# Kernel tuning notes

Hardware: AMD Instinct MI355X
Metric: run time of the kernel (lower is better)

Reference implementation:

```python
import jax, jax.numpy as jnp
import numpy as np

V = 2562
DEG = 8
NNZ = V * DEG
B, FIN, FOUT, K = 1, 8, 16, 5
X = Y = Z = 8


def setup_inputs() -> dict:
    key = jax.random.key(0)
    k1, k2, k3, k4, k5 = jax.random.split(key, 5)
    inputs = jax.random.normal(k1, (B, FIN, V, X, Y, Z), dtype=jnp.float32)
    # COO sparse Laplacian: each vertex has DEG entries (valid row indices)
    lap_rows = jnp.repeat(jnp.arange(V, dtype=jnp.int32), DEG)
    lap_cols = jax.random.randint(k2, (NNZ,), 0, V, dtype=jnp.int32)
    lap_vals = jax.random.normal(k3, (NNZ,), dtype=jnp.float32) * 0.1
    std = np.sqrt(2.0 / (FIN * K)).astype(np.float32)
    weight = jax.random.normal(k4, (K, FIN, FOUT), dtype=jnp.float32) * std
    bias = jnp.full((FOUT,), 0.01, dtype=jnp.float32)
    return {"inputs": inputs, "lap_rows": lap_rows, "lap_cols": lap_cols,
            "lap_vals": lap_vals, "weight": weight, "bias": bias}


def _spmv(vals, rows, cols, x):
    # sparse [V,V] @ dense [V,D] via gather + segment_sum
    return jax.ops.segment_sum(vals[:, None] * x[cols], rows, num_segments=V)


def reference(inputs, lap_rows, lap_cols, lap_vals, weight, bias):
    # x0: [V, Fin*B*X*Y*Z]
    x0 = jnp.transpose(inputs, (2, 1, 0, 3, 4, 5)).reshape(V, FIN * B * X * Y * Z)
    xs = [x0]
    if K > 1:
        x1 = _spmv(lap_vals, lap_rows, lap_cols, x0)
        xs.append(x1)
        for _ in range(2, K):
            x2 = 2.0 * _spmv(lap_vals, lap_rows, lap_cols, x1) - x0
            xs.append(x2)
            x0, x1 = x1, x2
    cheb = jnp.stack(xs, 0).reshape(K, V, FIN, B, X, Y, Z)
    # matmul over (K, Fin): out [B, Fout, V, X, Y, Z]
    out = jnp.einsum('kvfbxyz,kfo->bovxyz', cheb, weight)
    out = out + bias[None, :, None, None, None, None]
    return out
```

## Files before the change

### kernel.cpp

```cpp
#include <hip/hip_runtime.h>
#include <hip/hip_bf16.h>
#include <hip/hip_fp16.h>

constexpr int V_    = 2562;
constexpr int DEG_  = 8;
constexpr int FIN_  = 8;
constexpr int FOUT_ = 16;
constexpr int S_    = 512;
constexpr int VS_   = V_ * S_;
constexpr int VP_   = 2564;
constexpr int LSTR  = 12;
constexpr long INT_PLANE = (long)S_ * VP_;
constexpr int TPB   = 1024;
constexpr int NV    = 3;

__device__ __forceinline__ float4 ld4(const float* p) {
    return *reinterpret_cast<const float4*>(p);
}
__device__ __forceinline__ void st4(float* p, float4 v) {
    *reinterpret_cast<float4*>(p) = v;
}
__device__ __forceinline__ unsigned h2bits(__half2 h) {
    union { __half2 h; unsigned u; } c; c.h = h; return c.u;
}
__device__ __forceinline__ __half2 bits2h(unsigned u) {
    union { unsigned u; __half2 h; } c; c.u = u; return c.h;
}
__device__ __forceinline__ unsigned packh2(float e, float o) {
    return h2bits(__halves2half2(__float2half(e), __float2half(o)));
}

__global__ __launch_bounds__(256)
void transpose_k(const float* __restrict__ src, float* __restrict__ dst,
                 int M, int N, long srcZ, long dstZ, int dstStride)
{
    __shared__ float tile[64][65];
    const long zs = (long)blockIdx.z * srcZ;
    const long zd = (long)blockIdx.z * dstZ;
    const int n0 = blockIdx.x * 64;
    const int m0 = blockIdx.y * 64;
    const int t  = threadIdx.x;
    const int q  = t & 15;
    const int r  = t >> 4;

#pragma unroll
    for (int i = 0; i < 4; ++i) {
        const int m = m0 + r + i * 16;
        const int n = n0 + q * 4;
        if (m < M && n < N) {
            const float4 x = ld4(src + zs + (long)m * N + n);
            tile[r + i * 16][q * 4 + 0] = x.x;
            tile[r + i * 16][q * 4 + 1] = x.y;
            tile[r + i * 16][q * 4 + 2] = x.z;
            tile[r + i * 16][q * 4 + 3] = x.w;
        }
    }
    __syncthreads();
#pragma unroll
    for (int i = 0; i < 4; ++i) {
        const int n = n0 + r + i * 16;
        const int m = m0 + q * 4;
        if (n < N && (m + 4) <= dstStride) {
            const float4 x = make_float4(tile[q * 4 + 0][r + i * 16],
                                         tile[q * 4 + 1][r + i * 16],
                                         tile[q * 4 + 2][r + i * 16],
                                         tile[q * 4 + 3][r + i * 16]);
            st4(dst + zd + (long)n * dstStride + m, x);
        }
    }
}

__global__ __launch_bounds__(TPB)
void cheb_rec(const float* __restrict__ inT,
              const int*   __restrict__ cols,
              const float* __restrict__ vals,
              ushort* __restrict__ cheb)
{
    extern __shared__ unsigned cur[];
    const int s2 = blockIdx.x * 2;
    const int t  = threadIdx.x;

    {
        const int f  = t & 7;
        const int cb = t >> 3;
        const float* pe = inT + (long)f * INT_PLANE + (long)s2 * VP_;
        const float* po = pe + VP_;
        for (int c = cb; c < VP_ / 4; c += TPB / 8) {
            const float4 xe = ld4(pe + c * 4);
            const float4 xo = ld4(po + c * 4);
            cur[(c * 4 + 0) * LSTR + f] = packh2(xe.x, xo.x);
            cur[(c * 4 + 1) * LSTR + f] = packh2(xe.y, xo.y);
            cur[(c * 4 + 2) * LSTR + f] = packh2(xe.z, xo.z);
            cur[(c * 4 + 3) * LSTR + f] = packh2(xe.w, xo.w);
        }
    }
    __syncthreads();

    const __half2 two2 = __half2half2(__float2half(2.0f));

    __half2 xp[NV][8];
#pragma unroll
    for (int j = 0; j < NV; ++j) {
        const int v = (t + j * TPB < V_) ? (t + j * TPB) : 0;
        const uint4 lo = *reinterpret_cast<const uint4*>(&cur[v * LSTR]);
        const uint4 hi = *reinterpret_cast<const uint4*>(&cur[v * LSTR + 4]);
        xp[j][0] = bits2h(lo.x); xp[j][1] = bits2h(lo.y);
        xp[j][2] = bits2h(lo.z); xp[j][3] = bits2h(lo.w);
        xp[j][4] = bits2h(hi.x); xp[j][5] = bits2h(hi.y);
        xp[j][6] = bits2h(hi.z); xp[j][7] = bits2h(hi.w);
    }

#pragma unroll 1
    for (int k = 1; k < 5; ++k) {
        __half2 xk[NV][8];
#pragma unroll
        for (int j = 0; j < NV; ++j) {
            const bool valid = (t + j * TPB) < V_;
            const int v = valid ? (t + j * TPB) : 0;
            int off = v * 8;
            asm volatile("" : "+v"(off));
            const int4   ca = *reinterpret_cast<const int4*>(cols + off);
            const int4   cb = *reinterpret_cast<const int4*>(cols + off + 4);
            const float4 wa = ld4(vals + off);
            const float4 wb = ld4(vals + off + 4);
            const int   cc[8] = {ca.x, ca.y, ca.z, ca.w, cb.x, cb.y, cb.z, cb.w};
            const float ww[8] = {wa.x, wa.y, wa.z, wa.w, wb.x, wb.y, wb.z, wb.w};

            __half2 a[8];
#pragma unroll
            for (int e = 0; e < 8; ++e) a[e] = bits2h(0u);
#pragma unroll
            for (int n = 0; n < 8; ++n) {
                const unsigned* p = &cur[cc[n] * LSTR];
                const uint4 lo = *reinterpret_cast<const uint4*>(p);
                const uint4 hi = *reinterpret_cast<const uint4*>(p + 4);
                const __half2 w2 = __half2half2(__float2half(ww[n]));
                a[0] = __hfma2(w2, bits2h(lo.x), a[0]);
                a[1] = __hfma2(w2, bits2h(lo.y), a[1]);
                a[2] = __hfma2(w2, bits2h(lo.z), a[2]);
                a[3] = __hfma2(w2, bits2h(lo.w), a[3]);
                a[4] = __hfma2(w2, bits2h(hi.x), a[4]);
                a[5] = __hfma2(w2, bits2h(hi.y), a[5]);
                a[6] = __hfma2(w2, bits2h(hi.z), a[6]);
                a[7] = __hfma2(w2, bits2h(hi.w), a[7]);
            }
#pragma unroll
            for (int e = 0; e < 8; ++e)
                xk[j][e] = (k == 1) ? a[e]
                                    : __hfma2(two2, a[e], __hneg2(xp[j][e]));

            if (valid) {
                unsigned ue[4], uo[4];
#pragma unroll
                for (int i = 0; i < 4; ++i) {
                    const unsigned b0 = h2bits(xk[j][2 * i]);
                    const unsigned b1 = h2bits(xk[j][2 * i + 1]);
                    ue[i] = __builtin_amdgcn_perm(b1, b0, 0x05040100u);
                    uo[i] = __builtin_amdgcn_perm(b1, b0, 0x07060302u);
                }
                const long base = (((long)(k - 1) * S_ + s2) * V_ + v) * 8;
                *reinterpret_cast<uint4*>(cheb + base) =
                    make_uint4(ue[0], ue[1], ue[2], ue[3]);
                *reinterpret_cast<uint4*>(cheb + base + (long)V_ * 8) =
                    make_uint4(uo[0], uo[1], uo[2], uo[3]);
            }

            if (k < 4) {
                const uint4 lo = *reinterpret_cast<const uint4*>(&cur[v * LSTR]);
                const uint4 hi = *reinterpret_cast<const uint4*>(&cur[v * LSTR + 4]);
                xp[j][0] = bits2h(lo.x); xp[j][1] = bits2h(lo.y);
                xp[j][2] = bits2h(lo.z); xp[j][3] = bits2h(lo.w);
                xp[j][4] = bits2h(hi.x); xp[j][5] = bits2h(hi.y);
                xp[j][6] = bits2h(hi.z); xp[j][7] = bits2h(hi.w);
            }
        }
        if (k < 4) {
            __syncthreads();
#pragma unroll
            for (int j = 0; j < NV; ++j) {
                const int vr = t + j * TPB;
                if (vr < V_) {
                    *reinterpret_cast<uint4*>(&cur[vr * LSTR]) =
                        make_uint4(h2bits(xk[j][0]), h2bits(xk[j][1]),
                                   h2bits(xk[j][2]), h2bits(xk[j][3]));
                    *reinterpret_cast<uint4*>(&cur[vr * LSTR + 4]) =
                        make_uint4(h2bits(xk[j][4]), h2bits(xk[j][5]),
                                   h2bits(xk[j][6]), h2bits(xk[j][7]));
                }
            }
            __syncthreads();
        }
    }
}

__global__ __launch_bounds__(TPB)
void proj(const float* __restrict__ in,
          const ushort* __restrict__ cheb,
          const float* __restrict__ W,
          const float* __restrict__ bias,
          float* __restrict__ out)
{
    extern __shared__ float sm[];
    const int v0 = blockIdx.x * 64;
    const int s0 = blockIdx.y * 16;
    const int t  = threadIdx.x;

    const int tv = t & 63;
    const int ts = t >> 6;
    const int vg = (v0 + tv < V_) ? (v0 + tv) : (V_ - 1);

    int4 ck[4];
#pragma unroll
    for (int k = 0; k < 4; ++k)
        ck[k] = *reinterpret_cast<const int4*>(
            cheb + (((long)k * S_ + (s0 + ts)) * V_ + vg) * 8);

#pragma unroll
    for (int p = 0; p < 2; ++p) {
        const int idx = t + p * TPB;
        const int sq  = idx & 3;
        const int v   = (idx >> 2) & 63;
        const int f   = idx >> 8;
        const int vvg = (v0 + v < V_) ? (v0 + v) : (V_ - 1);
        const float4 x = ld4(in + (long)f * VS_ + (long)vvg * S_ + s0 + sq * 4);
        float* d = &sm[f * 1088 + v * 17 + sq * 4];
        d[0] = x.x; d[1] = x.y; d[2] = x.z; d[3] = x.w;
    }
    __syncthreads();

    float acc[16];
#pragma unroll
    for (int o = 0; o < 16; ++o) acc[o] = bias[o];

#pragma unroll
    for (int f = 0; f < FIN_; ++f) {
        const float xv = sm[f * 1088 + tv * 17 + ts];
#pragma unroll
        for (int o = 0; o < 16; ++o)
            acc[o] = fmaf(W[f * 16 + o], xv, acc[o]);
    }
#pragma unroll
    for (int k = 1; k < 5; ++k) {
        union { int4 q; __half u[8]; } pk;
        pk.q = ck[k - 1];
        float xv[8];
#pragma unroll
        for (int f = 0; f < 8; ++f)
            xv[f] = __half2float(pk.u[f]);
#pragma unroll
        for (int f = 0; f < 8; ++f) {
#pragma unroll
            for (int o = 0; o < 16; ++o)
                acc[o] = fmaf(W[(k * 8 + f) * 16 + o], xv[f], acc[o]);
        }
    }

    __syncthreads();
#pragma unroll
    for (int o = 0; o < 16; ++o)
        sm[o * 1088 + tv * 17 + ts] = acc[o];
    __syncthreads();
#pragma unroll
    for (int p = 0; p < 4; ++p) {
        const int idx = t + p * TPB;
        const int sq  = idx & 3;
        const int v   = (idx >> 2) & 63;
        const int o   = idx >> 8;
        if (v0 + v < V_) {
            const float* r = &sm[o * 1088 + v * 17 + sq * 4];
            st4(out + (long)o * VS_ + (long)(v0 + v) * S_ + s0 + sq * 4,
                make_float4(r[0], r[1], r[2], r[3]));
        }
    }
}

extern "C" void kernel_launch(void* const* d_in, const int* in_sizes, int n_in,
                              void* d_out, int out_size, void* d_ws, size_t ws_size,
                              hipStream_t stream) {
    const float* in   = (const float*)d_in[0];
    const int*   cols = (const int*)d_in[2];
    const float* vals = (const float*)d_in[3];
    const float* W    = (const float*)d_in[4];
    const float* bias = (const float*)d_in[5];
    float* out = (float*)d_out;

    float* inT = out;
    ushort* cheb = (ushort*)d_ws;

    (void)hipFuncSetAttribute((const void*)cheb_rec,
                              hipFuncAttributeMaxDynamicSharedMemorySize,
                              VP_ * LSTR * (int)sizeof(unsigned));
    (void)hipFuncSetAttribute((const void*)proj,
                              hipFuncAttributeMaxDynamicSharedMemorySize,
                              16 * 64 * 17 * (int)sizeof(float));

    transpose_k<<<dim3(8, 41, 8), 256, 0, stream>>>(
        in, inT, V_, S_, (long)VS_, INT_PLANE, VP_);

    cheb_rec<<<dim3(S_ / 2), TPB, VP_ * LSTR * (int)sizeof(unsigned), stream>>>(
        inT, cols, vals, cheb);

    proj<<<dim3(41, 32), TPB, 16 * 64 * 17 * (int)sizeof(float), stream>>>(
        in, cheb, W, bias, out);
}
```

Baseline: 199.9 us.

## Pack transposed input to fp16 pairs and feed x0 from cheb kernel to projection

The transpose kernel now writes fp16 half2-packed pairs of spatial columns instead of fp32, halving the intermediate buffer and removing the pack step in the recurrence kernel's load. When the workspace is large enough, the recurrence kernel also writes x0 in the same fp16 layout as the other Chebyshev terms. A new projection kernel then reads all five terms uniformly and skips the strided fp32 input gather through shared memory. The cost is an extra x0 write and x0 now being rounded to fp16 in the projection, which adds precision loss; a fallback keeps the old four-term path.

Measured after the change: 187.9 us. -6.0%, faster.

```diff
diff --git a/kernel.cpp b/kernel.cpp
--- a/kernel.cpp
+++ b/kernel.cpp
@@ -1,16 +1,16 @@
 #include <hip/hip_runtime.h>
-#include <hip/hip_bf16.h>
 #include <hip/hip_fp16.h>
 
 constexpr int V_    = 2562;
-constexpr int DEG_  = 8;
 constexpr int FIN_  = 8;
 constexpr int FOUT_ = 16;
 constexpr int S_    = 512;
+constexpr int SP_   = 256;
 constexpr int VS_   = V_ * S_;
 constexpr int VP_   = 2564;
 constexpr int LSTR  = 12;
-constexpr long INT_PLANE = (long)S_ * VP_;
+constexpr long PLH  = (long)SP_ * VP_;
+constexpr long PS   = (long)S_ * V_ * 8;
 constexpr int TPB   = 1024;
 constexpr int NV    = 3;
 
@@ -31,24 +31,23 @@
 }
 
 __global__ __launch_bounds__(256)
-void transpose_k(const float* __restrict__ src, float* __restrict__ dst,
-                 int M, int N, long srcZ, long dstZ, int dstStride)
+void transpose_pack(const float* __restrict__ src, unsigned* __restrict__ dst)
 {
     __shared__ float tile[64][65];
-    const long zs = (long)blockIdx.z * srcZ;
-    const long zd = (long)blockIdx.z * dstZ;
+    const int f  = blockIdx.z;
     const int n0 = blockIdx.x * 64;
     const int m0 = blockIdx.y * 64;
     const int t  = threadIdx.x;
     const int q  = t & 15;
     const int r  = t >> 4;
+    const float* sp_ = src + (long)f * VS_;
 
 #pragma unroll
     for (int i = 0; i < 4; ++i) {
         const int m = m0 + r + i * 16;
         const int n = n0 + q * 4;
-        if (m < M && n < N) {
-            const float4 x = ld4(src + zs + (long)m * N + n);
+        if (m < V_) {
+            const float4 x = ld4(sp_ + (long)m * S_ + n);
             tile[r + i * 16][q * 4 + 0] = x.x;
             tile[r + i * 16][q * 4 + 1] = x.y;
             tile[r + i * 16][q * 4 + 2] = x.z;
@@ -56,25 +55,32 @@
         }
     }
     __syncthreads();
-#pragma unroll
-    for (int i = 0; i < 4; ++i) {
-        const int n = n0 + r + i * 16;
-        const int m = m0 + q * 4;
-        if (n < N && (m + 4) <= dstStride) {
-            const float4 x = make_float4(tile[q * 4 + 0][r + i * 16],
-                                         tile[q * 4 + 1][r + i * 16],
-                                         tile[q * 4 + 2][r + i * 16],
-                                         tile[q * 4 + 3][r + i * 16]);
-            st4(dst + zd + (long)n * dstStride + m, x);
+
+#pragma unroll
+    for (int i = 0; i < 2; ++i) {
+        const int idx = t + i * 256;
+        const int vq  = idx & 15;
+        const int sp  = idx >> 4;
+        const int m   = m0 + vq * 4;
+        if (m + 4 <= VP_) {
+            unsigned u[4];
+#pragma unroll
+            for (int e = 0; e < 4; ++e)
+                u[e] = packh2(tile[vq * 4 + e][2 * sp],
+                              tile[vq * 4 + e][2 * sp + 1]);
+            *reinterpret_cast<uint4*>(
+                dst + (long)f * PLH + (long)(n0 / 2 + sp) * VP_ + m) =
+                make_uint4(u[0], u[1], u[2], u[3]);
         }
     }
 }
 
 __global__ __launch_bounds__(TPB)
-void cheb_rec(const float* __restrict__ inT,
+void cheb_rec(const unsigned* __restrict__ inTh,
               const int*   __restrict__ cols,
               const float* __restrict__ vals,
-              ushort* __restrict__ cheb)
+              ushort* __restrict__ chebX1,
+              ushort* __restrict__ x0p)
 {
     extern __shared__ unsigned cur[];
     const int s2 = blockIdx.x * 2;
@@ -83,18 +89,40 @@
     {
         const int f  = t & 7;
         const int cb = t >> 3;
-        const float* pe = inT + (long)f * INT_PLANE + (long)s2 * VP_;
-        const float* po = pe + VP_;
+        const unsigned* pl = inTh + (long)f * PLH + (long)blockIdx.x * VP_;
         for (int c = cb; c < VP_ / 4; c += TPB / 8) {
-            const float4 xe = ld4(pe + c * 4);
-            const float4 xo = ld4(po + c * 4);
-            cur[(c * 4 + 0) * LSTR + f] = packh2(xe.x, xo.x);
-            cur[(c * 4 + 1) * LSTR + f] = packh2(xe.y, xo.y);
-            cur[(c * 4 + 2) * LSTR + f] = packh2(xe.z, xo.z);
-            cur[(c * 4 + 3) * LSTR + f] = packh2(xe.w, xo.w);
-        }
-    }
-    __syncthreads();
+            const uint4 u = *reinterpret_cast<const uint4*>(pl + c * 4);
+            cur[(c * 4 + 0) * LSTR + f] = u.x;
+            cur[(c * 4 + 1) * LSTR + f] = u.y;
+            cur[(c * 4 + 2) * LSTR + f] = u.z;
+            cur[(c * 4 + 3) * LSTR + f] = u.w;
+        }
+    }
+    __syncthreads();
+
+    if (x0p) {
+#pragma unroll
+        for (int j = 0; j < NV; ++j) {
+            const int v = t + j * TPB;
+            if (v < V_) {
+                const uint4 lo = *reinterpret_cast<const uint4*>(&cur[v * LSTR]);
+                const uint4 hi = *reinterpret_cast<const uint4*>(&cur[v * LSTR + 4]);
+                const unsigned p0[4] = { lo.x, lo.z, hi.x, hi.z };
+                const unsigned p1[4] = { lo.y, lo.w, hi.y, hi.w };
+                unsigned ue[4], uo[4];
+#pragma unroll
+                for (int i = 0; i < 4; ++i) {
+                    ue[i] = __builtin_amdgcn_perm(p1[i], p0[i], 0x05040100u);
+                    uo[i] = __builtin_amdgcn_perm(p1[i], p0[i], 0x07060302u);
+                }
+                const long base = ((long)s2 * V_ + v) * 8;
+                *reinterpret_cast<uint4*>(x0p + base) =
+                    make_uint4(ue[0], ue[1], ue[2], ue[3]);
+                *reinterpret_cast<uint4*>(x0p + base + (long)V_ * 8) =
+                    make_uint4(uo[0], uo[1], uo[2], uo[3]);
+            }
+        }
+    }
 
     const __half2 two2 = __half2half2(__float2half(2.0f));
 
@@ -159,9 +187,9 @@
                     uo[i] = __builtin_amdgcn_perm(b1, b0, 0x07060302u);
                 }
                 const long base = (((long)(k - 1) * S_ + s2) * V_ + v) * 8;
-                *reinterpret_cast<uint4*>(cheb + base) =
+                *reinterpret_cast<uint4*>(chebX1 + base) =
                     make_uint4(ue[0], ue[1], ue[2], ue[3]);
-                *reinterpret_cast<uint4*>(cheb + base + (long)V_ * 8) =
+                *reinterpret_cast<uint4*>(chebX1 + base + (long)V_ * 8) =
                     make_uint4(uo[0], uo[1], uo[2], uo[3]);
             }
 
@@ -194,26 +222,83 @@
 }
 
 __global__ __launch_bounds__(TPB)
-void proj(const float* __restrict__ in,
-          const ushort* __restrict__ cheb,
-          const float* __restrict__ W,
-          const float* __restrict__ bias,
-          float* __restrict__ out)
+void proj5(const ushort* __restrict__ cheb,
+           const float* __restrict__ W,
+           const float* __restrict__ bias,
+           float* __restrict__ out)
 {
     extern __shared__ float sm[];
     const int v0 = blockIdx.x * 64;
     const int s0 = blockIdx.y * 16;
     const int t  = threadIdx.x;
-
     const int tv = t & 63;
     const int ts = t >> 6;
     const int vg = (v0 + tv < V_) ? (v0 + tv) : (V_ - 1);
 
+    int4 ck[5];
+#pragma unroll
+    for (int k = 0; k < 5; ++k)
+        ck[k] = *reinterpret_cast<const int4*>(
+            cheb + (long)k * PS + ((long)(s0 + ts) * V_ + vg) * 8);
+
+    float acc[16];
+#pragma unroll
+    for (int o = 0; o < 16; ++o) acc[o] = bias[o];
+
+#pragma unroll
+    for (int k = 0; k < 5; ++k) {
+        union { int4 q; __half u[8]; } pk;
+        pk.q = ck[k];
+        float xf[8];
+#pragma unroll
+        for (int f = 0; f < 8; ++f)
+            xf[f] = __half2float(pk.u[f]);
+#pragma unroll
+        for (int f = 0; f < 8; ++f) {
+#pragma unroll
+            for (int o = 0; o < 16; ++o)
+                acc[o] = fmaf(W[(k * 8 + f) * 16 + o], xf[f], acc[o]);
+        }
+    }
+
+#pragma unroll
+    for (int o = 0; o < 16; ++o)
+        sm[o * 1088 + tv * 17 + ts] = acc[o];
+    __syncthreads();
+#pragma unroll
+    for (int p = 0; p < 4; ++p) {
+        const int idx = t + p * TPB;
+        const int sq  = idx & 3;
+        const int v   = (idx >> 2) & 63;
+        const int o   = idx >> 8;
+        if (v0 + v < V_) {
+            const float* r = &sm[o * 1088 + v * 17 + sq * 4];
+            st4(out + (long)o * VS_ + (long)(v0 + v) * S_ + s0 + sq * 4,
+                make_float4(r[0], r[1], r[2], r[3]));
+        }
+    }
+}
+
+__global__ __launch_bounds__(TPB)
+void proj4(const float* __restrict__ in,
+           const ushort* __restrict__ cheb,
+           const float* __restrict__ W,
+           const float* __restrict__ bias,
+           float* __restrict__ out)
+{
+    extern __shared__ float sm[];
+    const int v0 = blockIdx.x * 64;
+    const int s0 = blockIdx.y * 16;
+    const int t  = threadIdx.x;
+    const int tv = t & 63;
+    const int ts = t >> 6;
+    const int vg = (v0 + tv < V_) ? (v0 + tv) : (V_ - 1);
+
     int4 ck[4];
 #pragma unroll
     for (int k = 0; k < 4; ++k)
         ck[k] = *reinterpret_cast<const int4*>(
-            cheb + (((long)k * S_ + (s0 + ts)) * V_ + vg) * 8);
+            cheb + (long)k * PS + ((long)(s0 + ts) * V_ + vg) * 8);
 
 #pragma unroll
     for (int p = 0; p < 2; ++p) {
@@ -243,15 +328,15 @@
     for (int k = 1; k < 5; ++k) {
         union { int4 q; __half u[8]; } pk;
         pk.q = ck[k - 1];
-        float xv[8];
+        float xf[8];
 #pragma unroll
         for (int f = 0; f < 8; ++f)
-            xv[f] = __half2float(pk.u[f]);
+            xf[f] = __half2float(pk.u[f]);
 #pragma unroll
         for (int f = 0; f < 8; ++f) {
 #pragma unroll
             for (int o = 0; o < 16; ++o)
-                acc[o] = fmaf(W[(k * 8 + f) * 16 + o], xv[f], acc[o]);
+                acc[o] = fmaf(W[(k * 8 + f) * 16 + o], xf[f], acc[o]);
         }
     }
 
@@ -284,22 +369,31 @@
     const float* bias = (const float*)d_in[5];
     float* out = (float*)d_out;
 
-    float* inT = out;
-    ushort* cheb = (ushort*)d_ws;
+    unsigned* inTh = (unsigned*)d_out;
+    const bool five = ws_size >= (size_t)(5 * PS * 2);
+    ushort* wsu    = (ushort*)d_ws;
+    ushort* x0p    = five ? wsu : nullptr;
+    ushort* chebX1 = five ? wsu + PS : wsu;
 
     (void)hipFuncSetAttribute((const void*)cheb_rec,
                               hipFuncAttributeMaxDynamicSharedMemorySize,
                               VP_ * LSTR * (int)sizeof(unsigned));
-    (void)hipFuncSetAttribute((const void*)proj,
+    (void)hipFuncSetAttribute((const void*)proj5,
                               hipFuncAttributeMaxDynamicSharedMemorySize,
                               16 * 64 * 17 * (int)sizeof(float));
-
-    transpose_k<<<dim3(8, 41, 8), 256, 0, stream>>>(
-        in, inT, V_, S_, (long)VS_, INT_PLANE, VP_);
-
-    cheb_rec<<<dim3(S_ / 2), TPB, VP_ * LSTR * (int)sizeof(unsigned), stream>>>(
-        inT, cols, vals, cheb);
-
-    proj<<<dim3(41, 32), TPB, 16 * 64 * 17 * (int)sizeof(float), stream>>>(
-        in, cheb, W, bias, out);
-}
+    (void)hipFuncSetAttribute((const void*)proj4,
+                              hipFuncAttributeMaxDynamicSharedMemorySize,
+                              16 * 64 * 17 * (int)sizeof(float));
+
+    transpose_pack<<<dim3(8, 41, 8), 256, 0, stream>>>(in, inTh);
+
+    cheb_rec<<<dim3(SP_), TPB, VP_ * LSTR * (int)sizeof(unsigned), stream>>>(
+        inTh, cols, vals, chebX1, x0p);
+
+    if (five)
+        proj5<<<dim3(41, 32), TPB, 16 * 64 * 17 * (int)sizeof(float), stream>>>(
+            wsu, W, bias, out);
+    else
+        proj4<<<dim3(41, 32), TPB, 16 * 64 * 17 * (int)sizeof(float), stream>>>(
+            in, chebX1, W, bias, out);
+}
```
